# Kernel tuning notes

Measured on AMD Instinct MI355X. Metric: run time of the kernel, lower is better.

The kernel has to match this reference:

```python
import jax, jax.numpy as jnp
import numpy as np

NUM_LAYERS = 3

def setup_inputs() -> dict:
    key = jax.random.key(0)
    ks = jax.random.split(key, 16)
    B = 8192
    NU, NI, D = 60000, 40000, 64
    N = NU + NI
    T_TRAIN, T_MAX = 128, 256
    E = 1600000
    return {
        "user_indices": jax.random.randint(ks[0], (B,), 0, NU, dtype=jnp.int32).astype(jnp.int64),
        "item_indices": jax.random.randint(ks[1], (B,), 0, NI, dtype=jnp.int32).astype(jnp.int64),
        "time_diffs": jax.random.randint(ks[2], (B,), 0, T_TRAIN, dtype=jnp.int32).astype(jnp.int64),
        "user_trends": jax.random.normal(ks[3], (B, T_TRAIN), dtype=jnp.float32),
        "item_trends": jax.random.normal(ks[4], (B, T_TRAIN), dtype=jnp.float32),
        "user_emb_table": 0.01 * jax.random.normal(ks[5], (NU, D), dtype=jnp.float32),
        "item_emb_table": 0.01 * jax.random.normal(ks[6], (NI, D), dtype=jnp.float32),
        "user_time_table": 0.01 * jax.random.normal(ks[7], (NU, T_MAX), dtype=jnp.float32),
        "item_time_table": 0.01 * jax.random.normal(ks[8], (NI, T_MAX), dtype=jnp.float32),
        "W1": 0.05 * jax.random.normal(ks[9], (T_TRAIN, 32), dtype=jnp.float32),
        "b1": jnp.zeros((32,), dtype=jnp.float32),
        "W2": 0.05 * jax.random.normal(ks[10], (32, T_MAX - T_TRAIN), dtype=jnp.float32),
        "b2": jnp.zeros((T_MAX - T_TRAIN,), dtype=jnp.float32),
        "edge_src": jax.random.randint(ks[11], (E,), 0, N, dtype=jnp.int32),
        "edge_dst": jax.random.randint(ks[12], (E,), 0, N, dtype=jnp.int32),
    }


def _graph_forward(user_emb_table, item_emb_table, edge_src, edge_dst):
    # LightGCN-style: mean of in-neighbor source features, num_layers hops,
    # then average over [input, layer1, ..., layerL] embeddings.
    N = user_emb_table.shape[0] + item_emb_table.shape[0]
    emb = jnp.concatenate([user_emb_table, item_emb_table], axis=0)  # [N, D]
    deg = jax.ops.segment_sum(jnp.ones_like(edge_dst, dtype=emb.dtype), edge_dst, num_segments=N)
    inv_deg = jnp.where(deg > 0, 1.0 / jnp.maximum(deg, 1.0), 0.0)[:, None]  # zero for isolated nodes (DGL mean -> 0)
    acc = emb
    cur = emb
    for _ in range(NUM_LAYERS):
        msgs = cur[edge_src]  # [E, D] gather
        summed = jax.ops.segment_sum(msgs, edge_dst, num_segments=N)
        cur = summed * inv_deg
        acc = acc + cur
    final = acc / jnp.asarray(NUM_LAYERS + 1, emb.dtype)
    return final[: user_emb_table.shape[0]], final[user_emb_table.shape[0]:]


def _mlp(t, W1, b1, W2, b2):
    # Linear->ReLU->Dropout(eval: identity)->Linear
    h = jax.nn.relu(t @ W1 + b1)
    return h @ W2 + b2


def reference(user_indices, item_indices, time_diffs, user_trends, item_trends,
              user_emb_table, item_emb_table, user_time_table, item_time_table,
              W1, b1, W2, b2, edge_src, edge_dst):
    user_embeddings, item_embeddings = _graph_forward(user_emb_table, item_emb_table, edge_src, edge_dst)
    ue = user_embeddings[user_indices]  # [B, D]
    ie = item_embeddings[item_indices]  # [B, D]
    global_match = jnp.sum(ue * ie, axis=-1)  # [B]

    ute = user_time_table[user_indices]  # [B, T_MAX]
    ite = item_time_table[item_indices]
    ut = jnp.concatenate([user_trends, _mlp(user_trends, W1, b1, W2, b2)], axis=1)  # [B, T_MAX]
    it = jnp.concatenate([item_trends, _mlp(item_trends, W1, b1, W2, b2)], axis=1)
    user_time_match = jnp.sum(ute * ut, axis=-1)
    item_time_match = jnp.sum(ite * it, axis=-1)

    B = user_indices.shape[0]
    ue0 = user_emb_table[user_indices]
    ie0 = item_emb_table[item_indices]
    reg_loss = 0.5 * (jnp.sum(ue0 ** 2) + jnp.sum(ie0 ** 2) + jnp.sum(ute ** 2) + jnp.sum(ite ** 2)) / float(B)

    return (jax.nn.sigmoid(global_match), jax.nn.sigmoid(user_time_match + item_time_match), reg_loss)
```

## Files before the change

### kernel.cpp

```cpp
#include <hip/hip_runtime.h>
#include <math.h>


__device__ __forceinline__ float bf2f(unsigned short h) {
    return __uint_as_float((unsigned)h << 16);
}
__device__ __forceinline__ unsigned short f2bf(float f) {
    unsigned u = __float_as_uint(f);
    return (unsigned short)((u + 0x7fffu + ((u >> 16) & 1u)) >> 16);
}


__global__ void zero256_kernel(int* p) { p[threadIdx.x] = 0; }

__global__ __launch_bounds__(256) void bin2_kernel(
    const int* __restrict__ src, const int* __restrict__ dst,
    int* __restrict__ cursor2, unsigned long long* __restrict__ pairs2,
    int E, int cap) {
    __shared__ int lcnt[256];
    __shared__ int lbase[256];
    int tid = threadIdx.x;
    int base = blockIdx.x * 4096;
    lcnt[tid] = 0;
    __syncthreads();
    #pragma unroll
    for (int i = 0; i < 16; ++i) {
        int e = base + i * 256 + tid;
        if (e < E) atomicAdd(&lcnt[dst[e] >> 9], 1);
    }
    __syncthreads();
    int c = lcnt[tid];
    lbase[tid] = (c > 0) ? atomicAdd(&cursor2[tid], c) : 0;
    __syncthreads();
    lcnt[tid] = 0;
    __syncthreads();
    #pragma unroll
    for (int i = 0; i < 16; ++i) {
        int e = base + i * 256 + tid;
        if (e < E) {
            int d = dst[e], s = src[e];
            int b = d >> 9;
            int r = lbase[b] + atomicAdd(&lcnt[b], 1);
            if (r < cap)
                pairs2[(size_t)b * cap + r] =
                    ((unsigned long long)(unsigned)d << 32) | (unsigned)s;
        }
    }
}

__global__ __launch_bounds__(256) void sort3_kernel(
    const unsigned long long* __restrict__ pairs2,
    const int* __restrict__ cursor2,
    float* __restrict__ invd, int* __restrict__ csr, int NODE_N, int cap) {
    __shared__ int lcnt[512];
    int bin = blockIdx.x;
    int nodebase = bin << 9;
    int n = cursor2[bin];
    if (n > cap) n = cap;
    const unsigned long long* p = pairs2 + (size_t)bin * cap;
    int tid = threadIdx.x;

    lcnt[tid] = 0;
    lcnt[tid + 256] = 0;
    __syncthreads();
    for (int i = tid; i < n; i += 256) {
        unsigned long long pr = p[i];
        int d = (int)(pr >> 32), s = (int)(pr & 0xffffffffu);
        int pos = atomicAdd(&lcnt[d - nodebase], 1);
        if (pos < 64) csr[(size_t)d * 64 + pos] = s;
    }
    __syncthreads();
    #pragma unroll
    for (int t = 0; t < 2; ++t) {
        int j = tid + t * 256;
        int node = nodebase + j;
        if (node <= NODE_N) {
            int own = lcnt[j];
            invd[node] = (own > 0) ? 1.0f / (float)own : 0.0f;
            int d0 = (own < 64) ? own : 64;
            int pend = (own <= 32) ? 32 : 64;
            int* row = csr + (size_t)node * 64;
            for (int k = d0; k < pend; ++k) row[k] = NODE_N;
        }
    }
}


__global__ __launch_bounds__(256) void convq_kernel(
    const float* __restrict__ utab, const float* __restrict__ itab,
    unsigned short* __restrict__ fb, int total, int uElems,
    const int* __restrict__ uidx, const int* __restrict__ iidx,
    float* __restrict__ uacc, float* __restrict__ iacc, int B, int convBlocks) {
    if ((int)blockIdx.x < convBlocks) {
        int i = (blockIdx.x * 256 + threadIdx.x) * 4;
        if (i >= total + 64) return;
        ushort4 o;
        if (i < total) {
            const float* srcp = (i < uElems) ? (utab + i) : (itab + (i - uElems));
            float4 v = *(const float4*)srcp;
            o.x = f2bf(v.x); o.y = f2bf(v.y); o.z = f2bf(v.z); o.w = f2bf(v.w);
        } else {
            o.x = 0; o.y = 0; o.z = 0; o.w = 0;
        }
        *(ushort4*)(fb + i) = o;
    } else {
        int w = ((blockIdx.x - convBlocks) * 256 + threadIdx.x) >> 6;
        int lane = threadIdx.x & 63;
        if (w >= 2 * B) return;
        if (w < B) {
            uacc[(size_t)w * 64 + lane] = utab[(size_t)uidx[w] * 64 + lane];
        } else {
            int b = w - B;
            iacc[(size_t)b * 64 + lane] = itab[(size_t)iidx[b] * 64 + lane];
        }
    }
}


#define GATHER4(sv, gx, gy, gz, gw_)                                     \
    {                                                                    \
        ushort4 v_ = *(const ushort4*)(cur + (size_t)(sv) * 64 + 4 * cL);\
        gx += bf2f(v_.x); gy += bf2f(v_.y);                              \
        gz += bf2f(v_.z); gw_ += bf2f(v_.w);                             \
    }
#define RED2(x) { x += __shfl_xor(x, 16, 64); x += __shfl_xor(x, 32, 64); }

__device__ __forceinline__ void prop_body(
    const unsigned short* __restrict__ cur,
    const int* __restrict__ csr, const float* __restrict__ invd,
    unsigned short* __restrict__ nxt, int NP1, int w, int lane) {
    int n0 = 2 * w, n1 = 2 * w + 1;
    if (n0 >= NP1) return;
    bool v1 = (n1 < NP1);
    int n1c = v1 ? n1 : n0;
    int g = lane >> 4;
    int cL = lane & 15;
    const int* c0 = csr + (size_t)n0 * 64;
    const int* c1 = csr + (size_t)n1c * 64;
    float inv0 = invd[n0];
    float inv1 = v1 ? invd[n1c] : 0.f;
    int s0 = c0[g], s1 = c0[4 + g], s2 = c0[8 + g], s3 = c0[12 + g];
    int t0 = c1[g], t1 = c1[4 + g], t2 = c1[8 + g], t3 = c1[12 + g];

    float ax = 0.f, ay = 0.f, az = 0.f, aw = 0.f;
    float bx = 0.f, by = 0.f, bz = 0.f, bw = 0.f;
    float ex = 0.f, ey = 0.f, ez = 0.f, ew = 0.f;
    float fx = 0.f, fy = 0.f, fz = 0.f, fw = 0.f;
    GATHER4(s0, ax, ay, az, aw);
    GATHER4(s1, bx, by, bz, bw);
    GATHER4(t0, ex, ey, ez, ew);
    GATHER4(t1, fx, fy, fz, fw);
    GATHER4(s2, ax, ay, az, aw);
    GATHER4(s3, bx, by, bz, bw);
    GATHER4(t2, ex, ey, ez, ew);
    GATHER4(t3, fx, fy, fz, fw);

    int deg0 = (inv0 > 0.f) ? (int)(1.0f / inv0 + 0.5f) : 0;
    int deg1 = (inv1 > 0.f) ? (int)(1.0f / inv1 + 0.5f) : 0;
    if (deg0 > 16) {
        int s4 = c0[16 + g], s5 = c0[20 + g], s6 = c0[24 + g], s7 = c0[28 + g];
        GATHER4(s4, ax, ay, az, aw);
        GATHER4(s5, bx, by, bz, bw);
        GATHER4(s6, ax, ay, az, aw);
        GATHER4(s7, bx, by, bz, bw);
    }
    if (deg1 > 16) {
        int t4 = c1[16 + g], t5 = c1[20 + g], t6 = c1[24 + g], t7 = c1[28 + g];
        GATHER4(t4, ex, ey, ez, ew);
        GATHER4(t5, fx, fy, fz, fw);
        GATHER4(t6, ex, ey, ez, ew);
        GATHER4(t7, fx, fy, fz, fw);
    }
    if (deg0 > 32) {
        #pragma unroll
        for (int pb = 32; pb < 64; pb += 8) {
            int u0 = c0[pb + g], u1 = c0[pb + 4 + g];
            GATHER4(u0, ax, ay, az, aw);
            GATHER4(u1, bx, by, bz, bw);
        }
    }
    if (deg1 > 32) {
        #pragma unroll
        for (int pb = 32; pb < 64; pb += 8) {
            int u0 = c1[pb + g], u1 = c1[pb + 4 + g];
            GATHER4(u0, ex, ey, ez, ew);
            GATHER4(u1, fx, fy, fz, fw);
        }
    }
    ax += bx; ay += by; az += bz; aw += bw;
    ex += fx; ey += fy; ez += fz; ew += fw;
    RED2(ax); RED2(ay); RED2(az); RED2(aw);
    RED2(ex); RED2(ey); RED2(ez); RED2(ew);
    if (g == 0) {
        ushort4 o;
        o.x = f2bf(ax * inv0); o.y = f2bf(ay * inv0);
        o.z = f2bf(az * inv0); o.w = f2bf(aw * inv0);
        *(ushort4*)(nxt + (size_t)n0 * 64 + 4 * cL) = o;
    } else if (g == 1 && v1) {
        ushort4 o;
        o.x = f2bf(ex * inv1); o.y = f2bf(ey * inv1);
        o.z = f2bf(ez * inv1); o.w = f2bf(ew * inv1);
        *(ushort4*)(nxt + (size_t)n1c * 64 + 4 * cL) = o;
    }
}

__global__ __launch_bounds__(256) void prop_kernel(
    const unsigned short* __restrict__ cur,
    const int* __restrict__ csr, const float* __restrict__ invd,
    unsigned short* __restrict__ nxt, int NP1) {
    int w = (blockIdx.x * blockDim.x + threadIdx.x) >> 6;
    int lane = threadIdx.x & 63;
    prop_body(cur, csr, invd, nxt, NP1, w, lane);
}

__global__ __launch_bounds__(256) void prop2q_kernel(
    const unsigned short* __restrict__ cur,
    const int* __restrict__ csr, const float* __restrict__ invd,
    unsigned short* __restrict__ nxt, int NP1, int prop_waves,
    const int* __restrict__ uidx, const int* __restrict__ iidx,
    float* __restrict__ uacc, float* __restrict__ iacc, int B, int NU) {
    int w = (blockIdx.x * blockDim.x + threadIdx.x) >> 6;
    int lane = threadIdx.x & 63;
    if (w < prop_waves) {
        prop_body(cur, csr, invd, nxt, NP1, w, lane);
    } else {
        int qw = w - prop_waves;
        if (qw >= 2 * B) return;
        if (qw < B) {
            uacc[(size_t)qw * 64 + lane] += bf2f(cur[(size_t)uidx[qw] * 64 + lane]);
        } else {
            int b = qw - B;
            iacc[(size_t)b * 64 + lane] += bf2f(cur[((size_t)NU + iidx[b]) * 64 + lane]);
        }
    }
}

__global__ __launch_bounds__(256) void prop3q_kernel(
    const unsigned short* __restrict__ cur,
    const int* __restrict__ uidx, const int* __restrict__ iidx,
    const int* __restrict__ csr, const float* __restrict__ invd,
    float* __restrict__ uacc, float* __restrict__ iacc, int B, int NU) {
    int w = (blockIdx.x * blockDim.x + threadIdx.x) >> 6;
    if (w >= 2 * B) return;
    int lane = threadIdx.x & 63;
    int g = lane >> 4;
    int cL = lane & 15;
    int node;
    float* acc;
    if (w < B) { node = uidx[w]; acc = uacc + (size_t)w * 64; }
    else       { node = NU + iidx[w - B]; acc = iacc + (size_t)(w - B) * 64; }
    const int* cbase = csr + (size_t)node * 64;
    float inv = invd[node];
    int s0 = cbase[g], s1 = cbase[4 + g], s2 = cbase[8 + g], s3 = cbase[12 + g];
    float ax = 0.f, ay = 0.f, az = 0.f, aw = 0.f;
    float bx = 0.f, by = 0.f, bz = 0.f, bw = 0.f;
    GATHER4(s0, ax, ay, az, aw);
    GATHER4(s1, bx, by, bz, bw);
    GATHER4(s2, ax, ay, az, aw);
    GATHER4(s3, bx, by, bz, bw);
    int deg = (inv > 0.f) ? (int)(1.0f / inv + 0.5f) : 0;
    if (deg > 16) {
        int s4 = cbase[16 + g], s5 = cbase[20 + g], s6 = cbase[24 + g], s7 = cbase[28 + g];
        GATHER4(s4, ax, ay, az, aw);
        GATHER4(s5, bx, by, bz, bw);
        GATHER4(s6, ax, ay, az, aw);
        GATHER4(s7, bx, by, bz, bw);
    }
    if (deg > 32) {
        #pragma unroll
        for (int pb = 32; pb < 64; pb += 8) {
            int u0 = cbase[pb + g], u1 = cbase[pb + 4 + g];
            GATHER4(u0, ax, ay, az, aw);
            GATHER4(u1, bx, by, bz, bw);
        }
    }
    ax += bx; ay += by; az += bz; aw += bw;
    RED2(ax); RED2(ay); RED2(az); RED2(aw);
    if (g == 0) {
        ushort4 own = *(const ushort4*)(cur + (size_t)node * 64 + 4 * cL);
        float4 prev = *(float4*)(acc + 4 * cL);
        prev.x += bf2f(own.x) + ax * inv;
        prev.y += bf2f(own.y) + ay * inv;
        prev.z += bf2f(own.z) + az * inv;
        prev.w += bf2f(own.w) + aw * inv;
        *(float4*)(acc + 4 * cL) = prev;
    }
}


__global__ __launch_bounds__(256) void timedot_kernel(
    const int* __restrict__ uidx, const int* __restrict__ iidx,
    const float* __restrict__ utr, const float* __restrict__ itr,
    const float* __restrict__ utt, const float* __restrict__ itt,
    const float* __restrict__ utab, const float* __restrict__ itab,
    const float* __restrict__ W1, const float* __restrict__ b1,
    const float* __restrict__ W2, const float* __restrict__ b2,
    const float* __restrict__ uacc, const float* __restrict__ iacc,
    float* __restrict__ out0, float* __restrict__ out1,
    float* __restrict__ regpart, int B) {
    __shared__ float sh[4][320];
    int wid = threadIdx.x >> 6, lane = threadIdx.x & 63;
    int b = blockIdx.x * 4 + wid;
    bool valid = (b < B);
    int bb = valid ? b : (B - 1);

    float* tu = sh[wid];
    float* ti = tu + 128;
    float* hu = ti + 128;
    float* hi = hu + 32;

    tu[lane]      = utr[(size_t)bb * 128 + lane];
    tu[lane + 64] = utr[(size_t)bb * 128 + 64 + lane];
    ti[lane]      = itr[(size_t)bb * 128 + lane];
    ti[lane + 64] = itr[(size_t)bb * 128 + 64 + lane];
    __syncthreads();

    {
        int j = lane & 31;
        const float* t = (lane < 32) ? tu : ti;
        float acc = b1[j];
        #pragma unroll 8
        for (int k = 0; k < 128; ++k) acc += t[k] * W1[k * 32 + j];
        float* h = (lane < 32) ? hu : hi;
        h[j] = fmaxf(acc, 0.0f);
    }
    __syncthreads();

    float mu0 = b2[lane], mu1 = b2[64 + lane];
    float mi0 = b2[lane], mi1 = b2[64 + lane];
    #pragma unroll 8
    for (int j = 0; j < 32; ++j) {
        float w0 = W2[j * 128 + lane], w1 = W2[j * 128 + 64 + lane];
        float huj = hu[j], hij = hi[j];
        mu0 += huj * w0; mu1 += huj * w1;
        mi0 += hij * w0; mi1 += hij * w1;
    }

    int u = uidx[bb], it = iidx[bb];
    const float* uterow = utt + (size_t)u * 256;
    const float* iterow = itt + (size_t)it * 256;
    float ute0 = uterow[lane], ute1 = uterow[64 + lane], ute2 = uterow[128 + lane], ute3 = uterow[192 + lane];
    float ite0 = iterow[lane], ite1 = iterow[64 + lane], ite2 = iterow[128 + lane], ite3 = iterow[192 + lane];

    float utm = ute0 * tu[lane] + ute1 * tu[64 + lane] + ute2 * mu0 + ute3 * mu1;
    float itm = ite0 * ti[lane] + ite1 * ti[64 + lane] + ite2 * mi0 + ite3 * mi1;

    float ue0 = utab[(size_t)u * 64 + lane], ie0 = itab[(size_t)it * 64 + lane];
    float reg = ute0 * ute0 + ute1 * ute1 + ute2 * ute2 + ute3 * ute3
              + ite0 * ite0 + ite1 * ite1 + ite2 * ite2 + ite3 * ite3
              + ue0 * ue0 + ie0 * ie0;

    float dv = uacc[(size_t)bb * 64 + lane] * iacc[(size_t)bb * 64 + lane];

    float s = utm + itm;
    for (int o = 32; o; o >>= 1) {
        s   += __shfl_down(s, o, 64);
        reg += __shfl_down(reg, o, 64);
        dv  += __shfl_down(dv, o, 64);
    }
    if (lane == 0 && valid) {
        out0[b] = 1.0f / (1.0f + expf(-dv * (1.0f / 16.0f)));
        out1[b] = 1.0f / (1.0f + expf(-s));
        regpart[b] = reg;
    }
}

__global__ __launch_bounds__(256) void regreduce_kernel(
    const float* __restrict__ regpart, float* __restrict__ out2, int B) {
    __shared__ float sh[256];
    float s = 0.0f;
    for (int i = threadIdx.x; i < B; i += 256) s += regpart[i];
    sh[threadIdx.x] = s;
    __syncthreads();
    for (int o = 128; o; o >>= 1) {
        if (threadIdx.x < (unsigned)o) sh[threadIdx.x] += sh[threadIdx.x + o];
        __syncthreads();
    }
    if (threadIdx.x == 0) out2[0] = 0.5f * sh[0] / (float)B;
}

extern "C" void kernel_launch(void* const* d_in, const int* in_sizes, int n_in,
                              void* d_out, int out_size, void* d_ws, size_t ws_size,
                              hipStream_t stream) {
    const int*   uidx = (const int*)d_in[0];
    const int*   iidx = (const int*)d_in[1];
    const float* utr  = (const float*)d_in[3];
    const float* itr  = (const float*)d_in[4];
    const float* utab = (const float*)d_in[5];
    const float* itab = (const float*)d_in[6];
    const float* utt  = (const float*)d_in[7];
    const float* itt  = (const float*)d_in[8];
    const float* W1   = (const float*)d_in[9];
    const float* b1   = (const float*)d_in[10];
    const float* W2   = (const float*)d_in[11];
    const float* b2   = (const float*)d_in[12];
    const int*   esrc = (const int*)d_in[13];
    const int*   edst = (const int*)d_in[14];

    const int B  = in_sizes[0];
    const int H  = in_sizes[10];
    const int TT = in_sizes[9] / H;
    const int TM = TT + in_sizes[12];
    const int NU = in_sizes[7] / TM;
    const int NI = in_sizes[8] / TM;
    const int N  = NU + NI;
    const int E  = in_sizes[13];
    const int D  = 64;
    const int nbin = (N + 1 + 511) >> 9;
    const int cap = 12288;

    char* ws = (char*)d_ws;
    size_t o = 0;
    auto carve = [&](size_t bytes) -> char* {
        char* p = ws + o;
        o = (o + bytes + 255) & ~(size_t)255;
        return p;
    };
    unsigned short* fb0 = (unsigned short*)carve((size_t)(N + 1) * D * sizeof(unsigned short));
    size_t fb1Bytes = (size_t)(N + 1) * D * sizeof(unsigned short);
    size_t p2Bytes  = (size_t)256 * cap * sizeof(unsigned long long);
    unsigned short* fb1 = (unsigned short*)carve(fb1Bytes > p2Bytes ? fb1Bytes : p2Bytes);
    float* uacc    = (float*)carve((size_t)B * D * sizeof(float));
    float* iacc    = (float*)carve((size_t)B * D * sizeof(float));
    float* invd    = (float*)carve((size_t)(N + 2) * sizeof(float));
    int*   csr     = (int*)  carve((size_t)(N + 1) * 64 * sizeof(int));
    int*   cursor2 = (int*)  carve(256 * sizeof(int));
    float* regpart = (float*)carve((size_t)B * sizeof(float));
    (void)ws_size;

    unsigned long long* pairs2 = (unsigned long long*)fb1;

    float* out0 = (float*)d_out;
    float* out1 = out0 + B;
    float* out2 = out1 + B;

    zero256_kernel<<<1, 256, 0, stream>>>(cursor2);
    bin2_kernel<<<(E + 4095) / 4096, 256, 0, stream>>>(esrc, edst, cursor2, pairs2, E, cap);
    sort3_kernel<<<nbin, 256, 0, stream>>>(pairs2, cursor2, invd, csr, N, cap);

    const int convBlocks = ((N * D + 64) / 4 + 255) / 256;
    const int qBlocks = (2 * B * 64 + 255) / 256;
    convq_kernel<<<convBlocks + qBlocks, 256, 0, stream>>>(
        utab, itab, fb0, N * D, NU * D, uidx, iidx, uacc, iacc, B, convBlocks);

    const int NP1 = N + 1;
    const int prop_waves = (NP1 + 1) / 2;
    const int prop_blocks = (prop_waves * 64 + 255) / 256;
    const int p2q_blocks = ((prop_waves + 2 * B) * 64 + 255) / 256;
    prop_kernel<<<prop_blocks, 256, 0, stream>>>(fb0, csr, invd, fb1, NP1);
    prop2q_kernel<<<p2q_blocks, 256, 0, stream>>>(fb1, csr, invd, fb0, NP1, prop_waves,
                                                  uidx, iidx, uacc, iacc, B, NU);
    prop3q_kernel<<<qBlocks, 256, 0, stream>>>(fb0, uidx, iidx, csr, invd, uacc, iacc, B, NU);

    timedot_kernel<<<(B + 3) / 4, 256, 0, stream>>>(uidx, iidx, utr, itr, utt, itt, utab, itab,
                                                    W1, b1, W2, b2, uacc, iacc,
                                                    out0, out1, regpart, B);
    regreduce_kernel<<<1, 256, 0, stream>>>(regpart, out2, B);
}
```

Measured before the change: 160.9 us.

## Fuse third-hop gather and layer accumulation into timedot, drop query accumulators

Removes the separate query-accumulator gathers and the third propagation kernel. The final-layer neighbor aggregation and the sum over all layer embeddings are now recomputed per query inside timedot, reading the bf16 layer buffers directly. The regularisation reduction moves to a per-block atomicAdd into the output, and the zeroing of the cursor and output is folded into the conversion kernel. This cuts three launches and the uacc/iacc traffic, but timedot becomes heavier and the per-row memory reads in it become wider; the atomic float sum also makes the reg-loss order nondeterministic.

```diff
diff --git a/kernel.cpp b/kernel.cpp
--- a/kernel.cpp
+++ b/kernel.cpp
@@ -11,7 +11,28 @@
 }
 
 
-__global__ void zero256_kernel(int* p) { p[threadIdx.x] = 0; }
+__global__ __launch_bounds__(256) void conv_kernel(
+    const float* __restrict__ utab, const float* __restrict__ itab,
+    unsigned short* __restrict__ fb, int total, int uElems,
+    int* __restrict__ cursor2, float* __restrict__ out2, int convBlocks) {
+    if ((int)blockIdx.x == convBlocks) {
+        cursor2[threadIdx.x] = 0;
+        if (threadIdx.x == 0) out2[0] = 0.0f;
+        return;
+    }
+    int i = (blockIdx.x * 256 + threadIdx.x) * 4;
+    if (i >= total + 64) return;
+    ushort4 o;
+    if (i < total) {
+        const float* srcp = (i < uElems) ? (utab + i) : (itab + (i - uElems));
+        float4 v = *(const float4*)srcp;
+        o.x = f2bf(v.x); o.y = f2bf(v.y); o.z = f2bf(v.z); o.w = f2bf(v.w);
+    } else {
+        o.x = 0; o.y = 0; o.z = 0; o.w = 0;
+    }
+    *(ushort4*)(fb + i) = o;
+}
+
 
 __global__ __launch_bounds__(256) void bin2_kernel(
     const int* __restrict__ src, const int* __restrict__ dst,
@@ -47,6 +68,7 @@
         }
     }
 }
+
 
 __global__ __launch_bounds__(256) void sort3_kernel(
     const unsigned long long* __restrict__ pairs2,
@@ -86,49 +108,20 @@
 }
 
 
-__global__ __launch_bounds__(256) void convq_kernel(
-    const float* __restrict__ utab, const float* __restrict__ itab,
-    unsigned short* __restrict__ fb, int total, int uElems,
-    const int* __restrict__ uidx, const int* __restrict__ iidx,
-    float* __restrict__ uacc, float* __restrict__ iacc, int B, int convBlocks) {
-    if ((int)blockIdx.x < convBlocks) {
-        int i = (blockIdx.x * 256 + threadIdx.x) * 4;
-        if (i >= total + 64) return;
-        ushort4 o;
-        if (i < total) {
-            const float* srcp = (i < uElems) ? (utab + i) : (itab + (i - uElems));
-            float4 v = *(const float4*)srcp;
-            o.x = f2bf(v.x); o.y = f2bf(v.y); o.z = f2bf(v.z); o.w = f2bf(v.w);
-        } else {
-            o.x = 0; o.y = 0; o.z = 0; o.w = 0;
-        }
-        *(ushort4*)(fb + i) = o;
-    } else {
-        int w = ((blockIdx.x - convBlocks) * 256 + threadIdx.x) >> 6;
-        int lane = threadIdx.x & 63;
-        if (w >= 2 * B) return;
-        if (w < B) {
-            uacc[(size_t)w * 64 + lane] = utab[(size_t)uidx[w] * 64 + lane];
-        } else {
-            int b = w - B;
-            iacc[(size_t)b * 64 + lane] = itab[(size_t)iidx[b] * 64 + lane];
-        }
-    }
-}
-
-
-#define GATHER4(sv, gx, gy, gz, gw_)                                     \
-    {                                                                    \
-        ushort4 v_ = *(const ushort4*)(cur + (size_t)(sv) * 64 + 4 * cL);\
-        gx += bf2f(v_.x); gy += bf2f(v_.y);                              \
-        gz += bf2f(v_.z); gw_ += bf2f(v_.w);                             \
+#define GATHER4(buf, sv, gx, gy, gz, gw_)                                  \
+    {                                                                      \
+        ushort4 v_ = *(const ushort4*)((buf) + (size_t)(sv) * 64 + 4 * cL);\
+        gx += bf2f(v_.x); gy += bf2f(v_.y);                                \
+        gz += bf2f(v_.z); gw_ += bf2f(v_.w);                               \
     }
 #define RED2(x) { x += __shfl_xor(x, 16, 64); x += __shfl_xor(x, 32, 64); }
 
-__device__ __forceinline__ void prop_body(
+__global__ __launch_bounds__(256) void prop_kernel(
     const unsigned short* __restrict__ cur,
     const int* __restrict__ csr, const float* __restrict__ invd,
-    unsigned short* __restrict__ nxt, int NP1, int w, int lane) {
+    unsigned short* __restrict__ nxt, int NP1) {
+    int w = (blockIdx.x * blockDim.x + threadIdx.x) >> 6;
+    int lane = threadIdx.x & 63;
     int n0 = 2 * w, n1 = 2 * w + 1;
     if (n0 >= NP1) return;
     bool v1 = (n1 < NP1);
@@ -146,45 +139,45 @@
     float bx = 0.f, by = 0.f, bz = 0.f, bw = 0.f;
     float ex = 0.f, ey = 0.f, ez = 0.f, ew = 0.f;
     float fx = 0.f, fy = 0.f, fz = 0.f, fw = 0.f;
-    GATHER4(s0, ax, ay, az, aw);
-    GATHER4(s1, bx, by, bz, bw);
-    GATHER4(t0, ex, ey, ez, ew);
-    GATHER4(t1, fx, fy, fz, fw);
-    GATHER4(s2, ax, ay, az, aw);
-    GATHER4(s3, bx, by, bz, bw);
-    GATHER4(t2, ex, ey, ez, ew);
-    GATHER4(t3, fx, fy, fz, fw);
+    GATHER4(cur, s0, ax, ay, az, aw);
+    GATHER4(cur, s1, bx, by, bz, bw);
+    GATHER4(cur, t0, ex, ey, ez, ew);
+    GATHER4(cur, t1, fx, fy, fz, fw);
+    GATHER4(cur, s2, ax, ay, az, aw);
+    GATHER4(cur, s3, bx, by, bz, bw);
+    GATHER4(cur, t2, ex, ey, ez, ew);
+    GATHER4(cur, t3, fx, fy, fz, fw);
 
     int deg0 = (inv0 > 0.f) ? (int)(1.0f / inv0 + 0.5f) : 0;
     int deg1 = (inv1 > 0.f) ? (int)(1.0f / inv1 + 0.5f) : 0;
     if (deg0 > 16) {
         int s4 = c0[16 + g], s5 = c0[20 + g], s6 = c0[24 + g], s7 = c0[28 + g];
-        GATHER4(s4, ax, ay, az, aw);
-        GATHER4(s5, bx, by, bz, bw);
-        GATHER4(s6, ax, ay, az, aw);
-        GATHER4(s7, bx, by, bz, bw);
+        GATHER4(cur, s4, ax, ay, az, aw);
+        GATHER4(cur, s5, bx, by, bz, bw);
+        GATHER4(cur, s6, ax, ay, az, aw);
+        GATHER4(cur, s7, bx, by, bz, bw);
     }
     if (deg1 > 16) {
         int t4 = c1[16 + g], t5 = c1[20 + g], t6 = c1[24 + g], t7 = c1[28 + g];
-        GATHER4(t4, ex, ey, ez, ew);
-        GATHER4(t5, fx, fy, fz, fw);
-        GATHER4(t6, ex, ey, ez, ew);
-        GATHER4(t7, fx, fy, fz, fw);
+        GATHER4(cur, t4, ex, ey, ez, ew);
+        GATHER4(cur, t5, fx, fy, fz, fw);
+        GATHER4(cur, t6, ex, ey, ez, ew);
+        GATHER4(cur, t7, fx, fy, fz, fw);
     }
     if (deg0 > 32) {
         #pragma unroll
         for (int pb = 32; pb < 64; pb += 8) {
             int u0 = c0[pb + g], u1 = c0[pb + 4 + g];
-            GATHER4(u0, ax, ay, az, aw);
-            GATHER4(u1, bx, by, bz, bw);
+            GATHER4(cur, u0, ax, ay, az, aw);
+            GATHER4(cur, u1, bx, by, bz, bw);
         }
     }
     if (deg1 > 32) {
         #pragma unroll
         for (int pb = 32; pb < 64; pb += 8) {
             int u0 = c1[pb + g], u1 = c1[pb + 4 + g];
-            GATHER4(u0, ex, ey, ez, ew);
-            GATHER4(u1, fx, fy, fz, fw);
+            GATHER4(cur, u0, ex, ey, ez, ew);
+            GATHER4(cur, u1, fx, fy, fz, fw);
         }
     }
     ax += bx; ay += by; az += bz; aw += bw;
@@ -204,89 +197,6 @@
     }
 }
 
-__global__ __launch_bounds__(256) void prop_kernel(
-    const unsigned short* __restrict__ cur,
-    const int* __restrict__ csr, const float* __restrict__ invd,
-    unsigned short* __restrict__ nxt, int NP1) {
-    int w = (blockIdx.x * blockDim.x + threadIdx.x) >> 6;
-    int lane = threadIdx.x & 63;
-    prop_body(cur, csr, invd, nxt, NP1, w, lane);
-}
-
-__global__ __launch_bounds__(256) void prop2q_kernel(
-    const unsigned short* __restrict__ cur,
-    const int* __restrict__ csr, const float* __restrict__ invd,
-    unsigned short* __restrict__ nxt, int NP1, int prop_waves,
-    const int* __restrict__ uidx, const int* __restrict__ iidx,
-    float* __restrict__ uacc, float* __restrict__ iacc, int B, int NU) {
-    int w = (blockIdx.x * blockDim.x + threadIdx.x) >> 6;
-    int lane = threadIdx.x & 63;
-    if (w < prop_waves) {
-        prop_body(cur, csr, invd, nxt, NP1, w, lane);
-    } else {
-        int qw = w - prop_waves;
-        if (qw >= 2 * B) return;
-        if (qw < B) {
-            uacc[(size_t)qw * 64 + lane] += bf2f(cur[(size_t)uidx[qw] * 64 + lane]);
-        } else {
-            int b = qw - B;
-            iacc[(size_t)b * 64 + lane] += bf2f(cur[((size_t)NU + iidx[b]) * 64 + lane]);
-        }
-    }
-}
-
-__global__ __launch_bounds__(256) void prop3q_kernel(
-    const unsigned short* __restrict__ cur,
-    const int* __restrict__ uidx, const int* __restrict__ iidx,
-    const int* __restrict__ csr, const float* __restrict__ invd,
-    float* __restrict__ uacc, float* __restrict__ iacc, int B, int NU) {
-    int w = (blockIdx.x * blockDim.x + threadIdx.x) >> 6;
-    if (w >= 2 * B) return;
-    int lane = threadIdx.x & 63;
-    int g = lane >> 4;
-    int cL = lane & 15;
-    int node;
-    float* acc;
-    if (w < B) { node = uidx[w]; acc = uacc + (size_t)w * 64; }
-    else       { node = NU + iidx[w - B]; acc = iacc + (size_t)(w - B) * 64; }
-    const int* cbase = csr + (size_t)node * 64;
-    float inv = invd[node];
-    int s0 = cbase[g], s1 = cbase[4 + g], s2 = cbase[8 + g], s3 = cbase[12 + g];
-    float ax = 0.f, ay = 0.f, az = 0.f, aw = 0.f;
-    float bx = 0.f, by = 0.f, bz = 0.f, bw = 0.f;
-    GATHER4(s0, ax, ay, az, aw);
-    GATHER4(s1, bx, by, bz, bw);
-    GATHER4(s2, ax, ay, az, aw);
-    GATHER4(s3, bx, by, bz, bw);
-    int deg = (inv > 0.f) ? (int)(1.0f / inv + 0.5f) : 0;
-    if (deg > 16) {
-        int s4 = cbase[16 + g], s5 = cbase[20 + g], s6 = cbase[24 + g], s7 = cbase[28 + g];
-        GATHER4(s4, ax, ay, az, aw);
-        GATHER4(s5, bx, by, bz, bw);
-        GATHER4(s6, ax, ay, az, aw);
-        GATHER4(s7, bx, by, bz, bw);
-    }
-    if (deg > 32) {
-        #pragma unroll
-        for (int pb = 32; pb < 64; pb += 8) {
-            int u0 = cbase[pb + g], u1 = cbase[pb + 4 + g];
-            GATHER4(u0, ax, ay, az, aw);
-            GATHER4(u1, bx, by, bz, bw);
-        }
-    }
-    ax += bx; ay += by; az += bz; aw += bw;
-    RED2(ax); RED2(ay); RED2(az); RED2(aw);
-    if (g == 0) {
-        ushort4 own = *(const ushort4*)(cur + (size_t)node * 64 + 4 * cL);
-        float4 prev = *(float4*)(acc + 4 * cL);
-        prev.x += bf2f(own.x) + ax * inv;
-        prev.y += bf2f(own.y) + ay * inv;
-        prev.z += bf2f(own.z) + az * inv;
-        prev.w += bf2f(own.w) + aw * inv;
-        *(float4*)(acc + 4 * cL) = prev;
-    }
-}
-
 
 __global__ __launch_bounds__(256) void timedot_kernel(
     const int* __restrict__ uidx, const int* __restrict__ iidx,
@@ -295,10 +205,13 @@
     const float* __restrict__ utab, const float* __restrict__ itab,
     const float* __restrict__ W1, const float* __restrict__ b1,
     const float* __restrict__ W2, const float* __restrict__ b2,
-    const float* __restrict__ uacc, const float* __restrict__ iacc,
+    const unsigned short* __restrict__ fb2,
+    const unsigned short* __restrict__ fb1l,
+    const int* __restrict__ csr, const float* __restrict__ invd,
     float* __restrict__ out0, float* __restrict__ out1,
-    float* __restrict__ regpart, int B) {
+    float* __restrict__ out2, int B, int NU, float regScale) {
     __shared__ float sh[4][320];
+    __shared__ float rsh[4];
     int wid = threadIdx.x >> 6, lane = threadIdx.x & 63;
     int b = blockIdx.x * 4 + wid;
     bool valid = (b < B);
@@ -345,12 +258,86 @@
     float utm = ute0 * tu[lane] + ute1 * tu[64 + lane] + ute2 * mu0 + ute3 * mu1;
     float itm = ite0 * ti[lane] + ite1 * ti[64 + lane] + ite2 * mi0 + ite3 * mi1;
 
-    float ue0 = utab[(size_t)u * 64 + lane], ie0 = itab[(size_t)it * 64 + lane];
-    float reg = ute0 * ute0 + ute1 * ute1 + ute2 * ute2 + ute3 * ute3
-              + ite0 * ite0 + ite1 * ite1 + ite2 * ite2 + ite3 * ite3
-              + ue0 * ue0 + ie0 * ie0;
-
-    float dv = uacc[(size_t)bb * 64 + lane] * iacc[(size_t)bb * 64 + lane];
+    float regA = ute0 * ute0 + ute1 * ute1 + ute2 * ute2 + ute3 * ute3
+               + ite0 * ite0 + ite1 * ite1 + ite2 * ite2 + ite3 * ite3;
+
+    int g = lane >> 4;
+    int cL = lane & 15;
+    int nu_node = u;
+    int ni_node = NU + it;
+    const int* cu = csr + (size_t)nu_node * 64;
+    const int* ci = csr + (size_t)ni_node * 64;
+    float invU = invd[nu_node];
+    float invI = invd[ni_node];
+    int s0 = cu[g], s1 = cu[4 + g], s2 = cu[8 + g], s3 = cu[12 + g];
+    int s4 = cu[16 + g], s5 = cu[20 + g], s6 = cu[24 + g], s7 = cu[28 + g];
+    int t0 = ci[g], t1 = ci[4 + g], t2 = ci[8 + g], t3 = ci[12 + g];
+    int t4 = ci[16 + g], t5 = ci[20 + g], t6 = ci[24 + g], t7 = ci[28 + g];
+
+    float ax = 0.f, ay = 0.f, az = 0.f, aw = 0.f;
+    float bx = 0.f, by = 0.f, bz = 0.f, bw = 0.f;
+    float ex = 0.f, ey = 0.f, ez = 0.f, ew = 0.f;
+    float fx = 0.f, fy = 0.f, fz = 0.f, fw = 0.f;
+    GATHER4(fb2, s0, ax, ay, az, aw);
+    GATHER4(fb2, s1, bx, by, bz, bw);
+    GATHER4(fb2, t0, ex, ey, ez, ew);
+    GATHER4(fb2, t1, fx, fy, fz, fw);
+    GATHER4(fb2, s2, ax, ay, az, aw);
+    GATHER4(fb2, s3, bx, by, bz, bw);
+    GATHER4(fb2, t2, ex, ey, ez, ew);
+    GATHER4(fb2, t3, fx, fy, fz, fw);
+    GATHER4(fb2, s4, ax, ay, az, aw);
+    GATHER4(fb2, s5, bx, by, bz, bw);
+    GATHER4(fb2, t4, ex, ey, ez, ew);
+    GATHER4(fb2, t5, fx, fy, fz, fw);
+    GATHER4(fb2, s6, ax, ay, az, aw);
+    GATHER4(fb2, s7, bx, by, bz, bw);
+    GATHER4(fb2, t6, ex, ey, ez, ew);
+    GATHER4(fb2, t7, fx, fy, fz, fw);
+
+    int degU = (invU > 0.f) ? (int)(1.0f / invU + 0.5f) : 0;
+    int degI = (invI > 0.f) ? (int)(1.0f / invI + 0.5f) : 0;
+    if (degU > 32) {
+        #pragma unroll
+        for (int pb = 32; pb < 64; pb += 8) {
+            int u0 = cu[pb + g], u1 = cu[pb + 4 + g];
+            GATHER4(fb2, u0, ax, ay, az, aw);
+            GATHER4(fb2, u1, bx, by, bz, bw);
+        }
+    }
+    if (degI > 32) {
+        #pragma unroll
+        for (int pb = 32; pb < 64; pb += 8) {
+            int u0 = ci[pb + g], u1 = ci[pb + 4 + g];
+            GATHER4(fb2, u0, ex, ey, ez, ew);
+            GATHER4(fb2, u1, fx, fy, fz, fw);
+        }
+    }
+    ax += bx; ay += by; az += bz; aw += bw;
+    ex += fx; ey += fy; ez += fz; ew += fw;
+    RED2(ax); RED2(ay); RED2(az); RED2(aw);
+    RED2(ex); RED2(ey); RED2(ez); RED2(ew);
+
+    float4 l0u = *(const float4*)(utab + (size_t)nu_node * 64 + 4 * cL);
+    float4 l0i = *(const float4*)(itab + (size_t)it * 64 + 4 * cL);
+    ushort4 l1u = *(const ushort4*)(fb1l + (size_t)nu_node * 64 + 4 * cL);
+    ushort4 l1i = *(const ushort4*)(fb1l + (size_t)ni_node * 64 + 4 * cL);
+    ushort4 l2u = *(const ushort4*)(fb2 + (size_t)nu_node * 64 + 4 * cL);
+    ushort4 l2i = *(const ushort4*)(fb2 + (size_t)ni_node * 64 + 4 * cL);
+
+    float ue0_ = l0u.x + bf2f(l1u.x) + bf2f(l2u.x) + ax * invU;
+    float ue1_ = l0u.y + bf2f(l1u.y) + bf2f(l2u.y) + ay * invU;
+    float ue2_ = l0u.z + bf2f(l1u.z) + bf2f(l2u.z) + az * invU;
+    float ue3_ = l0u.w + bf2f(l1u.w) + bf2f(l2u.w) + aw * invU;
+    float ie0_ = l0i.x + bf2f(l1i.x) + bf2f(l2i.x) + ex * invI;
+    float ie1_ = l0i.y + bf2f(l1i.y) + bf2f(l2i.y) + ey * invI;
+    float ie2_ = l0i.z + bf2f(l1i.z) + bf2f(l2i.z) + ez * invI;
+    float ie3_ = l0i.w + bf2f(l1i.w) + bf2f(l2i.w) + ew * invI;
+
+    float dv = ue0_ * ie0_ + ue1_ * ie1_ + ue2_ * ie2_ + ue3_ * ie3_;
+    float regB = l0u.x * l0u.x + l0u.y * l0u.y + l0u.z * l0u.z + l0u.w * l0u.w
+               + l0i.x * l0i.x + l0i.y * l0i.y + l0i.z * l0i.z + l0i.w * l0i.w;
+    float reg = regA + 0.25f * regB;
 
     float s = utm + itm;
     for (int o = 32; o; o >>= 1) {
@@ -358,25 +345,18 @@
         reg += __shfl_down(reg, o, 64);
         dv  += __shfl_down(dv, o, 64);
     }
-    if (lane == 0 && valid) {
-        out0[b] = 1.0f / (1.0f + expf(-dv * (1.0f / 16.0f)));
-        out1[b] = 1.0f / (1.0f + expf(-s));
-        regpart[b] = reg;
-    }
-}
-
-__global__ __launch_bounds__(256) void regreduce_kernel(
-    const float* __restrict__ regpart, float* __restrict__ out2, int B) {
-    __shared__ float sh[256];
-    float s = 0.0f;
-    for (int i = threadIdx.x; i < B; i += 256) s += regpart[i];
-    sh[threadIdx.x] = s;
-    __syncthreads();
-    for (int o = 128; o; o >>= 1) {
-        if (threadIdx.x < (unsigned)o) sh[threadIdx.x] += sh[threadIdx.x + o];
-        __syncthreads();
-    }
-    if (threadIdx.x == 0) out2[0] = 0.5f * sh[0] / (float)B;
+    if (lane == 0) {
+        if (valid) {
+            out0[b] = 1.0f / (1.0f + expf(-dv * (1.0f / 64.0f)));
+            out1[b] = 1.0f / (1.0f + expf(-s));
+        }
+        rsh[wid] = valid ? reg : 0.0f;
+    }
+    __syncthreads();
+    if (threadIdx.x == 0) {
+        float blocksum = rsh[0] + rsh[1] + rsh[2] + rsh[3];
+        atomicAdd(out2, blocksum * regScale);
+    }
 }
 
 extern "C" void kernel_launch(void* const* d_in, const int* in_sizes, int n_in,
@@ -420,12 +400,9 @@
     size_t fb1Bytes = (size_t)(N + 1) * D * sizeof(unsigned short);
     size_t p2Bytes  = (size_t)256 * cap * sizeof(unsigned long long);
     unsigned short* fb1 = (unsigned short*)carve(fb1Bytes > p2Bytes ? fb1Bytes : p2Bytes);
-    float* uacc    = (float*)carve((size_t)B * D * sizeof(float));
-    float* iacc    = (float*)carve((size_t)B * D * sizeof(float));
     float* invd    = (float*)carve((size_t)(N + 2) * sizeof(float));
     int*   csr     = (int*)  carve((size_t)(N + 1) * 64 * sizeof(int));
     int*   cursor2 = (int*)  carve(256 * sizeof(int));
-    float* regpart = (float*)carve((size_t)B * sizeof(float));
     (void)ws_size;
 
     unsigned long long* pairs2 = (unsigned long long*)fb1;
@@ -434,26 +411,20 @@
     float* out1 = out0 + B;
     float* out2 = out1 + B;
 
-    zero256_kernel<<<1, 256, 0, stream>>>(cursor2);
+    const int convBlocks = ((N * D + 64) / 4 + 255) / 256;
+    conv_kernel<<<convBlocks + 1, 256, 0, stream>>>(
+        utab, itab, fb0, N * D, NU * D, cursor2, out2, convBlocks);
+
     bin2_kernel<<<(E + 4095) / 4096, 256, 0, stream>>>(esrc, edst, cursor2, pairs2, E, cap);
     sort3_kernel<<<nbin, 256, 0, stream>>>(pairs2, cursor2, invd, csr, N, cap);
-
-    const int convBlocks = ((N * D + 64) / 4 + 255) / 256;
-    const int qBlocks = (2 * B * 64 + 255) / 256;
-    convq_kernel<<<convBlocks + qBlocks, 256, 0, stream>>>(
-        utab, itab, fb0, N * D, NU * D, uidx, iidx, uacc, iacc, B, convBlocks);
 
     const int NP1 = N + 1;
     const int prop_waves = (NP1 + 1) / 2;
     const int prop_blocks = (prop_waves * 64 + 255) / 256;
-    const int p2q_blocks = ((prop_waves + 2 * B) * 64 + 255) / 256;
     prop_kernel<<<prop_blocks, 256, 0, stream>>>(fb0, csr, invd, fb1, NP1);
-    prop2q_kernel<<<p2q_blocks, 256, 0, stream>>>(fb1, csr, invd, fb0, NP1, prop_waves,
-                                                  uidx, iidx, uacc, iacc, B, NU);
-    prop3q_kernel<<<qBlocks, 256, 0, stream>>>(fb0, uidx, iidx, csr, invd, uacc, iacc, B, NU);
-
-    timedot_kernel<<<(B + 3) / 4, 256, 0, stream>>>(uidx, iidx, utr, itr, utt, itt, utab, itab,
-                                                    W1, b1, W2, b2, uacc, iacc,
-                                                    out0, out1, regpart, B);
-    regreduce_kernel<<<1, 256, 0, stream>>>(regpart, out2, B);
-}
+    prop_kernel<<<prop_blocks, 256, 0, stream>>>(fb1, csr, invd, fb0, NP1);
+
+    timedot_kernel<<<(B + 3) / 4, 256, 0, stream>>>(
+        uidx, iidx, utr, itr, utt, itt, utab, itab, W1, b1, W2, b2,
+        fb0, fb1, csr, invd, out0, out1, out2, B, NU, 0.5f / (float)B);
+}
```

Result: faster. 154.5 us (-4.0%).
